# Performance work log

Hardware: AMD Instinct MI355X
Metric: run time of the kernel (lower is better)

## Reference

```python
import jax, jax.numpy as jnp
import numpy as np

TOKENS = 1024
IN_W = 512
BLOCK = 256
OUT_W = 512
N_BLOCKS = 64
K = 2


def setup_inputs() -> dict:
    key = jax.random.key(0)
    ks = jax.random.split(key, 8)
    u = lambda k, s: jax.random.uniform(k, s, jnp.float32, -1.0, 1.0)
    return {
        "x": jax.random.normal(ks[0], (TOKENS, IN_W), jnp.float32),
        "noise": jax.random.normal(ks[1], (TOKENS, N_BLOCKS), jnp.float32),
        "w1s": u(ks[2], (N_BLOCKS, IN_W, BLOCK)),
        "b1s": u(ks[3], (N_BLOCKS, BLOCK)),
        "w2s": u(ks[4], (N_BLOCKS, BLOCK, OUT_W)),
        "b2s": u(ks[5], (N_BLOCKS, OUT_W)),
        "mixer": jnp.zeros((IN_W, N_BLOCKS), jnp.float32) + 0.01 * jax.random.normal(ks[6], (IN_W, N_BLOCKS), jnp.float32),
        "noise_controller": jnp.zeros((IN_W, N_BLOCKS), jnp.float32) + 0.01 * jax.random.normal(ks[7], (IN_W, N_BLOCKS), jnp.float32),
        "k": K,
    }


def reference(x, noise, w1s, b1s, w2s, b2s, mixer, noise_controller, k):
    # noisy routing logits: mixer_prod + randn * softplus(noise_prod)
    h_x = x @ mixer + noise * jax.nn.softplus(x @ noise_controller)  # [B, E]
    topk_vals, topk_idx = jax.lax.top_k(h_x, k)                       # [B, K]
    scores = jax.nn.softmax(topk_vals, axis=-1)                       # [B, K]
    # per-token expert weight gather (faithful to index_select semantics)
    gw1 = w1s[topk_idx]  # [B, K, I, H]
    gb1 = b1s[topk_idx]  # [B, K, H]
    gw2 = w2s[topk_idx]  # [B, K, H, O]
    gb2 = b2s[topk_idx]  # [B, K, O]
    v = jax.nn.relu(jnp.einsum('bi,bkih->bkh', x, gw1) + gb1)        # [B, K, H]
    out = jnp.einsum('bkh,bkho->bko', v, gw2) + gb2                   # [B, K, O]
    return jnp.sum(out * scores[..., None], axis=1)                   # [B, O]
```

## Files before the change

kernel.cpp:

```cpp
#include <hip/hip_runtime.h>
#include <math.h>

#define TOKENS    1024
#define IN_W      512
#define BLOCK_H   256
#define OUT_W     512
#define N_EXPERTS 64
#define TOPK      2
#define NSLOTS    (TOKENS * TOPK)
#define LIST_CAP  128
#define T_CAP     12
#define NGRP      8
#define XPAD      520
#define VPAD      264

__device__ __forceinline__ void red_xor(float4& v, int m) {
    v.x += __shfl_xor(v.x, m); v.y += __shfl_xor(v.y, m);
    v.z += __shfl_xor(v.z, m); v.w += __shfl_xor(v.w, m);
}

__device__ __forceinline__ void fma4(float4& a, float s, const float4& w) {
    a.x = fmaf(s, w.x, a.x); a.y = fmaf(s, w.y, a.y);
    a.z = fmaf(s, w.z, a.z); a.w = fmaf(s, w.w, a.w);
}

__global__ __launch_bounds__(256) void routing_kernel(
    const float* __restrict__ x, const float* __restrict__ noise,
    const float* __restrict__ mixer, const float* __restrict__ noisec,
    float* __restrict__ esc, int* __restrict__ counts, int* __restrict__ lists,
    float* __restrict__ out)
{
    __shared__ float xs[512];
    __shared__ float pm[4 * 64];
    __shared__ float pn[4 * 64];
    __shared__ float hs[64];
    const int t    = blockIdx.x;
    const int tid  = threadIdx.x;
    const int wave = tid >> 6, lane = tid & 63;
    const int rs   = lane >> 4;
    const int c    = lane & 15;

    if (tid < 128) {
        ((float4*)xs)[tid] = ((const float4*)(x + (size_t)t * IN_W))[tid];
        ((float4*)(out + (size_t)t * OUT_W))[tid] = make_float4(0.f, 0.f, 0.f, 0.f);
    }
    __syncthreads();

    float4 am = make_float4(0.f, 0.f, 0.f, 0.f), an = am;
    const float4* m4 = (const float4*)mixer;
    const float4* n4 = (const float4*)noisec;
    const int rbase = wave * 128;
    #pragma unroll 4
    for (int j = 0; j < 32; ++j) {
        const int r = rbase + j * 4 + rs;
        const float xv = xs[r];
        const float4 wm = m4[r * 16 + c];
        const float4 wn = n4[r * 16 + c];
        fma4(am, xv, wm);
        fma4(an, xv, wn);
    }
    red_xor(am, 16); red_xor(am, 32);
    red_xor(an, 16); red_xor(an, 32);
    if (lane < 16) {
        *(float4*)&pm[wave * 64 + lane * 4] = am;
        *(float4*)&pn[wave * 64 + lane * 4] = an;
    }
    __syncthreads();

    if (tid < 64) {
        const float am2 = pm[tid] + pm[64 + tid] + pm[128 + tid] + pm[192 + tid];
        const float an2 = pn[tid] + pn[64 + tid] + pn[128 + tid] + pn[192 + tid];
        const float sp = fmaxf(an2, 0.f) + log1pf(expf(-fabsf(an2)));
        hs[tid] = am2 + noise[(size_t)t * 64 + tid] * sp;
    }
    __syncthreads();

    if (tid == 0) {
        float b0 = -INFINITY, b1 = -INFINITY;
        int i0 = 0, i1 = 0;
        for (int i = 0; i < N_EXPERTS; ++i) {
            const float v = hs[i];
            if (v > b0)      { b1 = b0; i1 = i0; b0 = v; i0 = i; }
            else if (v > b1) { b1 = v; i1 = i; }
        }
        const float z   = expf(b1 - b0);
        const float inv = 1.f / (1.f + z);
        esc[t * 2 + 0] = inv;
        esc[t * 2 + 1] = z * inv;
        const int p0 = atomicAdd(&counts[i0], 1);
        if (p0 < LIST_CAP) lists[i0 * LIST_CAP + p0] = t * 2 + 0;
        const int p1 = atomicAdd(&counts[i1], 1);
        if (p1 < LIST_CAP) lists[i1 * LIST_CAP + p1] = t * 2 + 1;
    }
}

template<int T>
__device__ __forceinline__ void run_pass(
    int nTok, int wave, int lane,
    const float4* __restrict__ w1v, const float4* __restrict__ w2v,
    const float4* __restrict__ b1v, const float4* __restrict__ b2v,
    const float* __restrict__ xs, float* __restrict__ vsm,
    const int* __restrict__ slotIds, const float* __restrict__ escv,
    float* __restrict__ out)
{
    {
        const int c4l = lane & 3, r0 = lane >> 2;
        float4 acc[T];
        #pragma unroll
        for (int t = 0; t < T; ++t) acc[t] = make_float4(0.f, 0.f, 0.f, 0.f);
        const float4* wp = w1v + (size_t)(r0 * 64 + wave * 4 + c4l);
        const float*  xb = xs + r0;
        #pragma unroll 2
        for (int s = 0; s < 32; ++s) {
            const float4 w = wp[(size_t)s * 1024];
            #pragma unroll
            for (int t = 0; t < T; ++t) {
                const float xv = xb[t * XPAD + s * 16];
                acc[t].x = fmaf(xv, w.x, acc[t].x);
                acc[t].y = fmaf(xv, w.y, acc[t].y);
                acc[t].z = fmaf(xv, w.z, acc[t].z);
                acc[t].w = fmaf(xv, w.w, acc[t].w);
            }
        }
        #pragma unroll
        for (int t = 0; t < T; ++t) {
            red_xor(acc[t], 4); red_xor(acc[t], 8);
            red_xor(acc[t], 16); red_xor(acc[t], 32);
        }
        if (r0 == 0) {
            const float4 bb = b1v[wave * 4 + c4l];
            #pragma unroll
            for (int t = 0; t < T; ++t) {
                float4 r;
                r.x = fmaxf(acc[t].x + bb.x, 0.f);
                r.y = fmaxf(acc[t].y + bb.y, 0.f);
                r.z = fmaxf(acc[t].z + bb.z, 0.f);
                r.w = fmaxf(acc[t].w + bb.w, 0.f);
                *(float4*)&vsm[t * VPAD + wave * 16 + c4l * 4] = r;
            }
        }
    }
    __syncthreads();

    {
        const int c8 = lane & 7, r8 = lane >> 3;
        float4 acc[T];
        #pragma unroll
        for (int t = 0; t < T; ++t) acc[t] = make_float4(0.f, 0.f, 0.f, 0.f);
        const float4* wp = w2v + (size_t)(r8 * 128 + wave * 8 + c8);
        const float*  vb = vsm + r8;
        #pragma unroll 2
        for (int s = 0; s < 32; ++s) {
            const float4 w = wp[(size_t)s * 1024];
            #pragma unroll
            for (int t = 0; t < T; ++t) {
                const float vv = vb[t * VPAD + s * 8];
                acc[t].x = fmaf(vv, w.x, acc[t].x);
                acc[t].y = fmaf(vv, w.y, acc[t].y);
                acc[t].z = fmaf(vv, w.z, acc[t].z);
                acc[t].w = fmaf(vv, w.w, acc[t].w);
            }
        }
        #pragma unroll
        for (int t = 0; t < T; ++t) {
            red_xor(acc[t], 8); red_xor(acc[t], 16); red_xor(acc[t], 32);
        }
        const float4 bb = b2v[wave * 8 + c8];
        #pragma unroll
        for (int t = 0; t < T; ++t) {
            if ((t & 7) == r8 && t < nTok) {
                const float sc = escv[t];
                float* o = out + (size_t)(slotIds[t] >> 1) * OUT_W
                               + (wave * 8 + c8) * 4;
                atomicAdd(o + 0, (acc[t].x + bb.x) * sc);
                atomicAdd(o + 1, (acc[t].y + bb.y) * sc);
                atomicAdd(o + 2, (acc[t].z + bb.z) * sc);
                atomicAdd(o + 3, (acc[t].w + bb.w) * sc);
            }
        }
    }
}

__global__ __launch_bounds__(1024, 4) void expert_kernel(
    const float* __restrict__ x,
    const float* __restrict__ w1s, const float* __restrict__ b1s,
    const float* __restrict__ w2s, const float* __restrict__ b2s,
    const int* __restrict__ counts, const int* __restrict__ lists,
    const float* __restrict__ esc, float* __restrict__ out)
{
    __shared__ __align__(16) float xs[T_CAP * XPAD];
    __shared__ __align__(16) float vsm[T_CAP * VPAD];
    __shared__ int   slotIds[T_CAP];
    __shared__ float escv[T_CAP];

    const int e  = blockIdx.x;
    const int g  = blockIdx.y;
    const int ne = min(counts[e], LIST_CAP);
    const int tid  = threadIdx.x;
    const int wave = tid >> 6, lane = tid & 63;

    const float4* w1v = (const float4*)(w1s + (size_t)e * IN_W * BLOCK_H);
    const float4* w2v = (const float4*)(w2s + (size_t)e * BLOCK_H * OUT_W);
    const float4* b1v = (const float4*)(b1s + (size_t)e * BLOCK_H);
    const float4* b2v = (const float4*)(b2s + (size_t)e * OUT_W);
    const float4* x4  = (const float4*)x;

    for (int s0 = g; s0 < ne; s0 += NGRP * T_CAP) {
        const int nTok  = min(T_CAP, (ne - s0 + NGRP - 1) / NGRP);
        const int Tpath = (nTok <= 4) ? 4 : (nTok <= 8) ? 8 : 12;

        if (tid < T_CAP) {
            int s = 0; float sc = 0.f;
            if (tid < nTok) { s = lists[e * LIST_CAP + s0 + tid * NGRP]; sc = esc[s]; }
            slotIds[tid] = s;
            escv[tid]    = sc;
        }
        __syncthreads();

        for (int idx = tid; idx < Tpath * 128; idx += 1024) {
            const int t = idx >> 7, q = idx & 127;
            float4 v = make_float4(0.f, 0.f, 0.f, 0.f);
            if (t < nTok) v = x4[(size_t)(slotIds[t] >> 1) * 128 + q];
            *(float4*)&xs[t * XPAD + q * 4] = v;
        }
        __syncthreads();

        if (nTok <= 4)
            run_pass<4>(nTok, wave, lane, w1v, w2v, b1v, b2v, xs, vsm, slotIds, escv, out);
        else if (nTok <= 8)
            run_pass<8>(nTok, wave, lane, w1v, w2v, b1v, b2v, xs, vsm, slotIds, escv, out);
        else
            run_pass<12>(nTok, wave, lane, w1v, w2v, b1v, b2v, xs, vsm, slotIds, escv, out);
        __syncthreads();
    }
}

extern "C" void kernel_launch(void* const* d_in, const int* in_sizes, int n_in,
                              void* d_out, int out_size, void* d_ws, size_t ws_size,
                              hipStream_t stream) {
    const float* x      = (const float*)d_in[0];
    const float* noise  = (const float*)d_in[1];
    const float* w1s    = (const float*)d_in[2];
    const float* b1s    = (const float*)d_in[3];
    const float* w2s    = (const float*)d_in[4];
    const float* b2s    = (const float*)d_in[5];
    const float* mixer  = (const float*)d_in[6];
    const float* noisec = (const float*)d_in[7];
    float* out = (float*)d_out;

    char* ws = (char*)d_ws;
    int*   counts = (int*)ws;                       ws += 256;
    float* esc    = (float*)ws;                     ws += NSLOTS * sizeof(float);
    int*   lists  = (int*)ws;

    hipMemsetAsync(counts, 0, 256, stream);

    routing_kernel<<<TOKENS, 256, 0, stream>>>(x, noise, mixer, noisec,
                                               esc, counts, lists, out);
    expert_kernel<<<dim3(N_EXPERTS, NGRP), 1024, 0, stream>>>(
        x, w1s, b1s, w2s, b2s, counts, lists, esc, out);
}
```

Before: 179.6 us.

## Size expert groups adaptively and vectorize activation loads with 4-row weight blocks

The number of token groups per expert is now derived from that expert's token count (up to 6), so blocks with no work exit early. Each group is capped at 8 tokens. The inner loops of both GEMV passes now assign each lane four consecutive weight rows, so a single float4 read from shared memory of x or v feeds four weight vectors. This cuts LDS instructions per FMA and removes the redundant weight re-reads caused by spreading too few tokens over 8 groups. In exchange, more weight registers are live, and experts with many tokens now have fewer blocks running in parallel.

Measured after the change: 182.5 us. About the same (+1.6%).

```diff
diff --git a/kernel.cpp b/kernel.cpp
--- a/kernel.cpp
+++ b/kernel.cpp
@@ -9,8 +9,8 @@
 #define TOPK      2
 #define NSLOTS    (TOKENS * TOPK)
 #define LIST_CAP  128
-#define T_CAP     12
-#define NGRP      8
+#define T_CAP     8
+#define NGRP_MAX  6
 #define XPAD      520
 #define VPAD      264
 
@@ -108,18 +108,21 @@
         float4 acc[T];
         #pragma unroll
         for (int t = 0; t < T; ++t) acc[t] = make_float4(0.f, 0.f, 0.f, 0.f);
-        const float4* wp = w1v + (size_t)(r0 * 64 + wave * 4 + c4l);
-        const float*  xb = xs + r0;
+        const float4* wp = w1v + (size_t)(r0 * 4) * 64 + wave * 4 + c4l;
+        const float*  xb = xs + r0 * 4;
         #pragma unroll 2
-        for (int s = 0; s < 32; ++s) {
-            const float4 w = wp[(size_t)s * 1024];
+        for (int j = 0; j < 8; ++j) {
+            const float4 wa = wp[(size_t)(j * 64 + 0) * 64];
+            const float4 wb = wp[(size_t)(j * 64 + 1) * 64];
+            const float4 wc = wp[(size_t)(j * 64 + 2) * 64];
+            const float4 wd = wp[(size_t)(j * 64 + 3) * 64];
             #pragma unroll
             for (int t = 0; t < T; ++t) {
-                const float xv = xb[t * XPAD + s * 16];
-                acc[t].x = fmaf(xv, w.x, acc[t].x);
-                acc[t].y = fmaf(xv, w.y, acc[t].y);
-                acc[t].z = fmaf(xv, w.z, acc[t].z);
-                acc[t].w = fmaf(xv, w.w, acc[t].w);
+                const float4 xv = *(const float4*)&xb[t * XPAD + j * 64];
+                fma4(acc[t], xv.x, wa);
+                fma4(acc[t], xv.y, wb);
+                fma4(acc[t], xv.z, wc);
+                fma4(acc[t], xv.w, wd);
             }
         }
         #pragma unroll
@@ -147,18 +150,21 @@
         float4 acc[T];
         #pragma unroll
         for (int t = 0; t < T; ++t) acc[t] = make_float4(0.f, 0.f, 0.f, 0.f);
-        const float4* wp = w2v + (size_t)(r8 * 128 + wave * 8 + c8);
-        const float*  vb = vsm + r8;
+        const float4* wp = w2v + (size_t)(r8 * 4) * 128 + wave * 8 + c8;
+        const float*  vb = vsm + r8 * 4;
         #pragma unroll 2
-        for (int s = 0; s < 32; ++s) {
-            const float4 w = wp[(size_t)s * 1024];
+        for (int j = 0; j < 8; ++j) {
+            const float4 wa = wp[(size_t)(j * 32 + 0) * 128];
+            const float4 wb = wp[(size_t)(j * 32 + 1) * 128];
+            const float4 wc = wp[(size_t)(j * 32 + 2) * 128];
+            const float4 wd = wp[(size_t)(j * 32 + 3) * 128];
             #pragma unroll
             for (int t = 0; t < T; ++t) {
-                const float vv = vb[t * VPAD + s * 8];
-                acc[t].x = fmaf(vv, w.x, acc[t].x);
-                acc[t].y = fmaf(vv, w.y, acc[t].y);
-                acc[t].z = fmaf(vv, w.z, acc[t].z);
-                acc[t].w = fmaf(vv, w.w, acc[t].w);
+                const float4 vv = *(const float4*)&vb[t * VPAD + j * 32];
+                fma4(acc[t], vv.x, wa);
+                fma4(acc[t], vv.y, wb);
+                fma4(acc[t], vv.z, wc);
+                fma4(acc[t], vv.w, wd);
             }
         }
         #pragma unroll
@@ -196,6 +202,8 @@
     const int e  = blockIdx.x;
     const int g  = blockIdx.y;
     const int ne = min(counts[e], LIST_CAP);
+    const int G  = min(NGRP_MAX, (ne + T_CAP - 1) / T_CAP);
+    if (g >= G) return;
     const int tid  = threadIdx.x;
     const int wave = tid >> 6, lane = tid & 63;
 
@@ -205,13 +213,13 @@
     const float4* b2v = (const float4*)(b2s + (size_t)e * OUT_W);
     const float4* x4  = (const float4*)x;
 
-    for (int s0 = g; s0 < ne; s0 += NGRP * T_CAP) {
-        const int nTok  = min(T_CAP, (ne - s0 + NGRP - 1) / NGRP);
-        const int Tpath = (nTok <= 4) ? 4 : (nTok <= 8) ? 8 : 12;
+    for (int s0 = g; s0 < ne; s0 += G * T_CAP) {
+        const int nTok  = min(T_CAP, (ne - s0 + G - 1) / G);
+        const int Tpath = (nTok <= 4) ? 4 : 8;
 
         if (tid < T_CAP) {
             int s = 0; float sc = 0.f;
-            if (tid < nTok) { s = lists[e * LIST_CAP + s0 + tid * NGRP]; sc = esc[s]; }
+            if (tid < nTok) { s = lists[e * LIST_CAP + s0 + tid * G]; sc = esc[s]; }
             slotIds[tid] = s;
             escv[tid]    = sc;
         }
@@ -227,10 +235,8 @@
 
         if (nTok <= 4)
             run_pass<4>(nTok, wave, lane, w1v, w2v, b1v, b2v, xs, vsm, slotIds, escv, out);
-        else if (nTok <= 8)
+        else
             run_pass<8>(nTok, wave, lane, w1v, w2v, b1v, b2v, xs, vsm, slotIds, escv, out);
-        else
-            run_pass<12>(nTok, wave, lane, w1v, w2v, b1v, b2v, xs, vsm, slotIds, escv, out);
         __syncthreads();
     }
 }
@@ -257,6 +263,6 @@
 
     routing_kernel<<<TOKENS, 256, 0, stream>>>(x, noise, mixer, noisec,
                                                esc, counts, lists, out);
-    expert_kernel<<<dim3(N_EXPERTS, NGRP), 1024, 0, stream>>>(
+    expert_kernel<<<dim3(N_EXPERTS, NGRP_MAX), 1024, 0, stream>>>(
         x, w1s, b1s, w2s, b2s, counts, lists, esc, out);
 }
```
